# Optimization experiments

Measured on AMD Instinct MI355X. Metric: run time of the kernel, lower is better.

The kernel has to match this reference:

```python
import jax, jax.numpy as jnp
import numpy as np

GRID_SIZE = 5
GRID_RANGE = (-1.0, 1.0)


def setup_inputs() -> dict:
    key = jax.random.key(0)
    k1, k2, k3 = jax.random.split(key, 3)
    B, D, U, K = 16384, 1024, 128, GRID_SIZE + 3  # spline_order=3
    x = jax.random.normal(k1, (B, D), dtype=jnp.float32)
    # glorot-ish scale for weights
    base_weight = jax.random.normal(k2, (D, U), dtype=jnp.float32) * (1.0 / np.sqrt(D))
    spline_weight = jax.random.normal(k3, (D, U, K), dtype=jnp.float32) * (1.0 / np.sqrt(D))
    return {"x": x, "base_weight": base_weight, "spline_weight": spline_weight}


def reference(x, base_weight, spline_weight):
    # base path: SiLU(x @ W_b)
    base_out = jax.nn.silu(x @ base_weight)  # [B, U]
    # spline path: RBF over grid centers, then contract (note: x_norm in the
    # original call() is computed but unused, so it is omitted here)
    centers = jnp.linspace(GRID_RANGE[0], GRID_RANGE[1], GRID_SIZE)  # [G]
    dist = jnp.square(x[..., None] - centers)        # [B, D, G]
    rbf = jnp.exp(-5.0 * dist)                        # [B, D, G]
    spline_out = jnp.einsum('big,iug->bu', rbf, spline_weight[:, :, :GRID_SIZE])
    return base_out + spline_out
```

## Files before the change

### kernel.cpp

```cpp
#include <hip/hip_runtime.h>

typedef unsigned short u16;
typedef unsigned int u32;
typedef __bf16 bf16x8 __attribute__((ext_vector_type(8)));
typedef float f32x16 __attribute__((ext_vector_type(16)));

#define C2 (-7.213475204444817f)
#define T1C 0.28650480f
#define T2C 0.0067379470f

__device__ __forceinline__ u16 f2bf(float f) {
  u32 u = __float_as_uint(f);
  return (u16)((u + 0x7FFFu + ((u >> 16) & 1u)) >> 16);
}

__device__ __forceinline__ f32x16 mfma16(uint4 a, uint4 b, f32x16 c) {
  return __builtin_amdgcn_mfma_f32_32x32x16_bf16(
      __builtin_bit_cast(bf16x8, a), __builtin_bit_cast(bf16x8, b), c, 0, 0, 0);
}

__global__ __launch_bounds__(256) void kan_prep(const float* __restrict__ wb,
                                                const float* __restrict__ ws,
                                                u16* __restrict__ wst3) {
  __shared__ u16 tile[6][16][130];
  const int t = threadIdx.x;
  const int c = blockIdx.x;
#pragma unroll
  for (int it = 0; it < 8; ++it) {
    int idx = it * 256 + t;
    int d = idx >> 7, u = idx & 127;
    size_t base = (size_t)(c * 16 + d) * 128 + u;
    const float* p = ws + base * 8;
    float4 v0 = *(const float4*)p;
    float g4 = p[4];
    tile[0][d][u] = f2bf(v0.x);
    tile[1][d][u] = f2bf(v0.y);
    tile[2][d][u] = f2bf(v0.z);
    tile[3][d][u] = f2bf(v0.w);
    tile[4][d][u] = f2bf(g4);
    tile[5][d][u] = f2bf(wb[base]);
  }
  __syncthreads();
#pragma unroll
  for (int i = 0; i < 6; ++i) {
    int g = i * 256 + t;
    int s = g >> 8, r = g & 255;
    int nq = r >> 6, l = r & 63;
    int u = nq * 32 + (l & 31);
    int dbase = (l >> 5) * 8;
    u32 q[4];
#pragma unroll
    for (int j = 0; j < 4; ++j) {
      u32 lo = tile[s][dbase + 2 * j][u];
      u32 hi = tile[s][dbase + 2 * j + 1][u];
      q[j] = lo | (hi << 16);
    }
    uint4 w4; w4.x = q[0]; w4.y = q[1]; w4.z = q[2]; w4.w = q[3];
    *(uint4*)(wst3 + (size_t)c * 12288 + (size_t)g * 8) = w4;
  }
}

__global__ __launch_bounds__(512, 2) void kan_main(const float* __restrict__ x,
                                                   const u16* __restrict__ wst3,
                                                   float* __restrict__ out) {
  __shared__ __align__(16) char lds[98304];

  const int t = threadIdx.x;
  const int lane = t & 63;
  const int w = t >> 6;
  const int kq = w & 3;
  const int wn = w >> 2;
  const int b0 = blockIdx.x * 64;

  f32x16 acc[8];
#pragma unroll
  for (int i = 0; i < 8; ++i)
#pragma unroll
    for (int j = 0; j < 16; ++j) acc[i][j] = 0.f;

  const int r = t >> 3, o = t & 7;
  const float* xp = x + (size_t)(b0 + r) * 1024 + o * 8;
  const u32 aw = (u32)((((r >> 5) * 4 + (o >> 1)) << 10) + ((o & 1) << 9) +
                       (((r & 31) ^ o) << 4));

  const char* bsrc = (const char*)wst3 + kq * 24576 + wn * 2048 + lane * 16;

  const u32 ar = (u32)((kq << 10) + ((lane >> 5) << 9) +
                       ((((lane & 31) ^ (kq * 2 + (lane >> 5)))) << 4));

  auto rbf_write = [&](char* buf, float4 xa, float4 xb) {
    float xf[8] = {xa.x, xa.y, xa.z, xa.w, xb.x, xb.y, xb.z, xb.w};
    u32 pk[6][4];
#pragma unroll
    for (int pp = 0; pp < 4; ++pp) {
      u32 lo6[6], hi6[6];
#pragma unroll
      for (int e = 0; e < 2; ++e) {
        float xv = xf[2 * pp + e];
        float t0 = C2 * xv;
        float P = __builtin_amdgcn_exp2f(t0 * xv);
        float Qp = __builtin_amdgcn_exp2f(-t0);
        float Qm = __builtin_amdgcn_exp2f(t0);
        float PQ = P * Qp, PQm = P * Qm;
        u32* dst = e ? hi6 : lo6;
        dst[0] = __float_as_uint(PQm * Qm * T2C) + 0x8000u;
        dst[1] = __float_as_uint(PQm * T1C) + 0x8000u;
        dst[2] = __float_as_uint(P) + 0x8000u;
        dst[3] = __float_as_uint(PQ * T1C) + 0x8000u;
        dst[4] = __float_as_uint(PQ * Qp * T2C) + 0x8000u;
        dst[5] = __float_as_uint(xv) + 0x8000u;
      }
#pragma unroll
      for (int s = 0; s < 6; ++s)
        pk[s][pp] = __builtin_amdgcn_perm(hi6[s], lo6[s], 0x07060302);
    }
#pragma unroll
    for (int s = 0; s < 6; ++s) {
      uint4 v; v.x = pk[s][0]; v.y = pk[s][1]; v.z = pk[s][2]; v.w = pk[s][3];
      *(uint4*)(buf + s * 8192 + aw) = v;
    }
  };

  float4 xc0 = *(const float4*)(xp);
  float4 xc1 = *(const float4*)(xp + 4);
  rbf_write(lds, xc0, xc1);
  xc0 = *(const float4*)(xp + 64);
  xc1 = *(const float4*)(xp + 68);
  __syncthreads();

  for (int i = 0; i < 16; ++i) {
    char* cur = lds + (size_t)(i & 1) * 49152;
    char* nxt = lds + (size_t)((i + 1) & 1) * 49152;
    const char* bc = bsrc + (size_t)i * 98304;

    uint4 av[6], bv[6];
#pragma unroll
    for (int s = 0; s < 3; ++s) {
      bv[2 * s] = *(const uint4*)(bc + s * 4096);
      bv[2 * s + 1] = *(const uint4*)(bc + s * 4096 + 1024);
      av[2 * s] = *(const uint4*)(cur + s * 8192 + ar);
      av[2 * s + 1] = *(const uint4*)(cur + s * 8192 + 4096 + ar);
    }
    if (i < 15) {
      rbf_write(nxt, xc0, xc1);
      if (i < 14) {
        xc0 = *(const float4*)(xp + (i + 2) * 64);
        xc1 = *(const float4*)(xp + (i + 2) * 64 + 4);
      }
    }
#pragma unroll
    for (int s = 0; s < 3; ++s) {
      acc[0] = mfma16(av[2 * s], bv[2 * s], acc[0]);
      acc[1] = mfma16(av[2 * s], bv[2 * s + 1], acc[1]);
      acc[2] = mfma16(av[2 * s + 1], bv[2 * s], acc[2]);
      acc[3] = mfma16(av[2 * s + 1], bv[2 * s + 1], acc[3]);
    }
#pragma unroll
    for (int s = 3; s < 6; ++s) {
      int j = 2 * (s - 3);
      bv[j] = *(const uint4*)(bc + s * 4096);
      bv[j + 1] = *(const uint4*)(bc + s * 4096 + 1024);
      av[j] = *(const uint4*)(cur + s * 8192 + ar);
      av[j + 1] = *(const uint4*)(cur + s * 8192 + 4096 + ar);
    }
#pragma unroll
    for (int s = 3; s < 5; ++s) {
      int j = 2 * (s - 3);
      acc[0] = mfma16(av[j], bv[j], acc[0]);
      acc[1] = mfma16(av[j], bv[j + 1], acc[1]);
      acc[2] = mfma16(av[j + 1], bv[j], acc[2]);
      acc[3] = mfma16(av[j + 1], bv[j + 1], acc[3]);
    }
    acc[4] = mfma16(av[4], bv[4], acc[4]);
    acc[5] = mfma16(av[4], bv[5], acc[5]);
    acc[6] = mfma16(av[5], bv[4], acc[6]);
    acc[7] = mfma16(av[5], bv[5], acc[7]);
    __syncthreads();
  }

#pragma unroll
  for (int q = 0; q < 4; ++q) {
    if (kq != 0) {
      char* slab = lds + ((kq - 1) * 2 + wn) * 8192;
#pragma unroll
      for (int rq = 0; rq < 4; ++rq) {
        *(float4*)(slab + rq * 1024 + lane * 16) =
            make_float4(acc[q][4 * rq], acc[q][4 * rq + 1],
                        acc[q][4 * rq + 2], acc[q][4 * rq + 3]);
        *(float4*)(slab + 4096 + rq * 1024 + lane * 16) =
            make_float4(acc[4 + q][4 * rq], acc[4 + q][4 * rq + 1],
                        acc[4 + q][4 * rq + 2], acc[4 + q][4 * rq + 3]);
      }
    }
    __syncthreads();
    if (kq == 0) {
#pragma unroll
      for (int p = 1; p < 4; ++p) {
        const char* slab = lds + ((p - 1) * 2 + wn) * 8192;
#pragma unroll
        for (int rq = 0; rq < 4; ++rq) {
          float4 vs = *(const float4*)(slab + rq * 1024 + lane * 16);
          float4 vb = *(const float4*)(slab + 4096 + rq * 1024 + lane * 16);
          acc[q][4 * rq] += vs.x; acc[q][4 * rq + 1] += vs.y;
          acc[q][4 * rq + 2] += vs.z; acc[q][4 * rq + 3] += vs.w;
          acc[4 + q][4 * rq] += vb.x; acc[4 + q][4 * rq + 1] += vb.y;
          acc[4 + q][4 * rq + 2] += vb.z; acc[4 + q][4 * rq + 3] += vb.w;
        }
      }
      const int col = wn * 64 + (q & 1) * 32 + (lane & 31);
#pragma unroll
      for (int reg = 0; reg < 16; ++reg) {
        int row = (q >> 1) * 32 + (reg & 3) + 8 * (reg >> 2) + 4 * (lane >> 5);
        float z = acc[4 + q][reg];
        float sv = z / (1.0f + __expf(-z));
        out[(size_t)(b0 + row) * 128 + col] = sv + acc[q][reg];
      }
    }
    __syncthreads();
  }
}

extern "C" void kernel_launch(void* const* d_in, const int* in_sizes, int n_in,
                              void* d_out, int out_size, void* d_ws, size_t ws_size,
                              hipStream_t stream) {
  const float* x  = (const float*)d_in[0];
  const float* wb = (const float*)d_in[1];
  const float* ws = (const float*)d_in[2];
  u16* wst3 = (u16*)d_ws;
  float* out = (float*)d_out;

  kan_prep<<<dim3(64), 256, 0, stream>>>(wb, ws, wst3);
  kan_main<<<dim3(256), 512, 0, stream>>>(x, wst3, out);
}
```

Baseline: 137.3 us.

## Halve batch tile to 32 rows per block for more occupancy and staggered compute

Shrinks each block's batch tile from 64 to 32 rows, halving accumulators and LDS (48 KB) and doubling the grid to 512 blocks, with launch bounds raised to 4 blocks per CU. The MFMA inner loop becomes a software-pipelined chain that prefetches the next A/B fragments, and the two wave groups run the RBF generation and the GEMM in opposite order so VALU and matrix work overlap. This targets latency hiding through higher occupancy. The cost is that each block re-reads the full weight stream from global/L2 for half as many rows, so weight traffic per output doubles, and the tighter register budget may cause spills.

```diff
diff --git a/kernel.cpp b/kernel.cpp
--- a/kernel.cpp
+++ b/kernel.cpp
@@ -60,45 +60,45 @@
   }
 }
 
-__global__ __launch_bounds__(512, 2) void kan_main(const float* __restrict__ x,
+__global__ __launch_bounds__(512, 4) void kan_main(const float* __restrict__ x,
                                                    const u16* __restrict__ wst3,
                                                    float* __restrict__ out) {
-  __shared__ __align__(16) char lds[98304];
+  __shared__ __align__(16) char lds[49152];
 
   const int t = threadIdx.x;
   const int lane = t & 63;
   const int w = t >> 6;
   const int kq = w & 3;
   const int wn = w >> 2;
-  const int b0 = blockIdx.x * 64;
-
-  f32x16 acc[8];
-#pragma unroll
-  for (int i = 0; i < 8; ++i)
+  const int b0 = blockIdx.x * 32;
+
+  f32x16 acc[4];
+#pragma unroll
+  for (int i = 0; i < 4; ++i)
 #pragma unroll
     for (int j = 0; j < 16; ++j) acc[i][j] = 0.f;
 
-  const int r = t >> 3, o = t & 7;
-  const float* xp = x + (size_t)(b0 + r) * 1024 + o * 8;
-  const u32 aw = (u32)((((r >> 5) * 4 + (o >> 1)) << 10) + ((o & 1) << 9) +
-                       (((r & 31) ^ o) << 4));
+  const int r = t >> 4, o4 = t & 15;
+  const float* xp = x + (size_t)(b0 + r) * 1024 + o4 * 4;
+  const u32 aw = ((u32)(o4 >> 2) << 10) + ((u32)((o4 >> 1) & 1) << 9) +
+                 ((u32)((r ^ (o4 >> 1)) & 31) << 4) + ((u32)(o4 & 1) << 3);
 
   const char* bsrc = (const char*)wst3 + kq * 24576 + wn * 2048 + lane * 16;
 
-  const u32 ar = (u32)((kq << 10) + ((lane >> 5) << 9) +
-                       ((((lane & 31) ^ (kq * 2 + (lane >> 5)))) << 4));
-
-  auto rbf_write = [&](char* buf, float4 xa, float4 xb) {
-    float xf[8] = {xa.x, xa.y, xa.z, xa.w, xb.x, xb.y, xb.z, xb.w};
-    u32 pk[6][4];
-#pragma unroll
-    for (int pp = 0; pp < 4; ++pp) {
+  const u32 ar = ((u32)kq << 10) + ((u32)(lane >> 5) << 9) +
+                 ((u32)((lane & 31) ^ (kq * 2 + (lane >> 5))) << 4);
+
+  auto rbf_write = [&](char* buf, float4 xv) {
+    float xf[4] = {xv.x, xv.y, xv.z, xv.w};
+    u32 pk[6][2];
+#pragma unroll
+    for (int pp = 0; pp < 2; ++pp) {
       u32 lo6[6], hi6[6];
 #pragma unroll
       for (int e = 0; e < 2; ++e) {
-        float xv = xf[2 * pp + e];
-        float t0 = C2 * xv;
-        float P = __builtin_amdgcn_exp2f(t0 * xv);
+        float v = xf[2 * pp + e];
+        float t0 = C2 * v;
+        float P = __builtin_amdgcn_exp2f(t0 * v);
         float Qp = __builtin_amdgcn_exp2f(-t0);
         float Qm = __builtin_amdgcn_exp2f(t0);
         float PQ = P * Qp, PQm = P * Qm;
@@ -108,7 +108,7 @@
         dst[2] = __float_as_uint(P) + 0x8000u;
         dst[3] = __float_as_uint(PQ * T1C) + 0x8000u;
         dst[4] = __float_as_uint(PQ * Qp * T2C) + 0x8000u;
-        dst[5] = __float_as_uint(xv) + 0x8000u;
+        dst[5] = __float_as_uint(v) + 0x8000u;
       }
 #pragma unroll
       for (int s = 0; s < 6; ++s)
@@ -116,70 +116,65 @@
     }
 #pragma unroll
     for (int s = 0; s < 6; ++s) {
-      uint4 v; v.x = pk[s][0]; v.y = pk[s][1]; v.z = pk[s][2]; v.w = pk[s][3];
-      *(uint4*)(buf + s * 8192 + aw) = v;
+      uint2 v2; v2.x = pk[s][0]; v2.y = pk[s][1];
+      *(uint2*)(buf + s * 4096 + aw) = v2;
     }
   };
 
-  float4 xc0 = *(const float4*)(xp);
-  float4 xc1 = *(const float4*)(xp + 4);
-  rbf_write(lds, xc0, xc1);
-  xc0 = *(const float4*)(xp + 64);
-  xc1 = *(const float4*)(xp + 68);
+  auto gemm_chain = [&](const char* cur, const char* bp) {
+    uint4 a0 = *(const uint4*)(cur + ar);
+    uint4 c0 = *(const uint4*)(bp);
+    uint4 c1 = *(const uint4*)(bp + 1024);
+    uint4 a1 = *(const uint4*)(cur + 4096 + ar);
+    uint4 c2 = *(const uint4*)(bp + 4096);
+    uint4 c3 = *(const uint4*)(bp + 4096 + 1024);
+#pragma unroll
+    for (int s = 0; s < 6; ++s) {
+      uint4 au = a0, b0 = c0, b1 = c1;
+      a0 = a1; c0 = c2; c1 = c3;
+      if (s < 4) {
+        a1 = *(const uint4*)(cur + (s + 2) * 4096 + ar);
+        c2 = *(const uint4*)(bp + (s + 2) * 4096);
+        c3 = *(const uint4*)(bp + (s + 2) * 4096 + 1024);
+      }
+      if (s < 5) {
+        acc[0] = mfma16(au, b0, acc[0]);
+        acc[1] = mfma16(au, b1, acc[1]);
+      } else {
+        acc[2] = mfma16(au, b0, acc[2]);
+        acc[3] = mfma16(au, b1, acc[3]);
+      }
+    }
+  };
+
+  float4 xc = *(const float4*)xp;
+  rbf_write(lds, xc);
+  xc = *(const float4*)(xp + 64);
   __syncthreads();
 
   for (int i = 0; i < 16; ++i) {
-    char* cur = lds + (size_t)(i & 1) * 49152;
-    char* nxt = lds + (size_t)((i + 1) & 1) * 49152;
+    char* cur = lds + (i & 1) * 24576;
+    char* nxt = lds + ((i + 1) & 1) * 24576;
     const char* bc = bsrc + (size_t)i * 98304;
 
-    uint4 av[6], bv[6];
-#pragma unroll
-    for (int s = 0; s < 3; ++s) {
-      bv[2 * s] = *(const uint4*)(bc + s * 4096);
-      bv[2 * s + 1] = *(const uint4*)(bc + s * 4096 + 1024);
-      av[2 * s] = *(const uint4*)(cur + s * 8192 + ar);
-      av[2 * s + 1] = *(const uint4*)(cur + s * 8192 + 4096 + ar);
-    }
-    if (i < 15) {
-      rbf_write(nxt, xc0, xc1);
-      if (i < 14) {
-        xc0 = *(const float4*)(xp + (i + 2) * 64);
-        xc1 = *(const float4*)(xp + (i + 2) * 64 + 4);
-      }
-    }
-#pragma unroll
-    for (int s = 0; s < 3; ++s) {
-      acc[0] = mfma16(av[2 * s], bv[2 * s], acc[0]);
-      acc[1] = mfma16(av[2 * s], bv[2 * s + 1], acc[1]);
-      acc[2] = mfma16(av[2 * s + 1], bv[2 * s], acc[2]);
-      acc[3] = mfma16(av[2 * s + 1], bv[2 * s + 1], acc[3]);
-    }
-#pragma unroll
-    for (int s = 3; s < 6; ++s) {
-      int j = 2 * (s - 3);
-      bv[j] = *(const uint4*)(bc + s * 4096);
-      bv[j + 1] = *(const uint4*)(bc + s * 4096 + 1024);
-      av[j] = *(const uint4*)(cur + s * 8192 + ar);
-      av[j + 1] = *(const uint4*)(cur + s * 8192 + 4096 + ar);
-    }
-#pragma unroll
-    for (int s = 3; s < 5; ++s) {
-      int j = 2 * (s - 3);
-      acc[0] = mfma16(av[j], bv[j], acc[0]);
-      acc[1] = mfma16(av[j], bv[j + 1], acc[1]);
-      acc[2] = mfma16(av[j + 1], bv[j], acc[2]);
-      acc[3] = mfma16(av[j + 1], bv[j + 1], acc[3]);
-    }
-    acc[4] = mfma16(av[4], bv[4], acc[4]);
-    acc[5] = mfma16(av[4], bv[5], acc[5]);
-    acc[6] = mfma16(av[5], bv[4], acc[6]);
-    acc[7] = mfma16(av[5], bv[5], acc[7]);
+    if (wn == 0) {
+      if (i < 15) {
+        rbf_write(nxt, xc);
+        if (i < 14) xc = *(const float4*)(xp + (i + 2) * 64);
+      }
+      gemm_chain(cur, bc);
+    } else {
+      gemm_chain(cur, bc);
+      if (i < 15) {
+        rbf_write(nxt, xc);
+        if (i < 14) xc = *(const float4*)(xp + (i + 2) * 64);
+      }
+    }
     __syncthreads();
   }
 
 #pragma unroll
-  for (int q = 0; q < 4; ++q) {
+  for (int q = 0; q < 2; ++q) {
     if (kq != 0) {
       char* slab = lds + ((kq - 1) * 2 + wn) * 8192;
 #pragma unroll
@@ -188,8 +183,8 @@
             make_float4(acc[q][4 * rq], acc[q][4 * rq + 1],
                         acc[q][4 * rq + 2], acc[q][4 * rq + 3]);
         *(float4*)(slab + 4096 + rq * 1024 + lane * 16) =
-            make_float4(acc[4 + q][4 * rq], acc[4 + q][4 * rq + 1],
-                        acc[4 + q][4 * rq + 2], acc[4 + q][4 * rq + 3]);
+            make_float4(acc[2 + q][4 * rq], acc[2 + q][4 * rq + 1],
+                        acc[2 + q][4 * rq + 2], acc[2 + q][4 * rq + 3]);
       }
     }
     __syncthreads();
@@ -203,15 +198,15 @@
           float4 vb = *(const float4*)(slab + 4096 + rq * 1024 + lane * 16);
           acc[q][4 * rq] += vs.x; acc[q][4 * rq + 1] += vs.y;
           acc[q][4 * rq + 2] += vs.z; acc[q][4 * rq + 3] += vs.w;
-          acc[4 + q][4 * rq] += vb.x; acc[4 + q][4 * rq + 1] += vb.y;
-          acc[4 + q][4 * rq + 2] += vb.z; acc[4 + q][4 * rq + 3] += vb.w;
+          acc[2 + q][4 * rq] += vb.x; acc[2 + q][4 * rq + 1] += vb.y;
+          acc[2 + q][4 * rq + 2] += vb.z; acc[2 + q][4 * rq + 3] += vb.w;
         }
       }
-      const int col = wn * 64 + (q & 1) * 32 + (lane & 31);
+      const int col = wn * 64 + q * 32 + (lane & 31);
 #pragma unroll
       for (int reg = 0; reg < 16; ++reg) {
-        int row = (q >> 1) * 32 + (reg & 3) + 8 * (reg >> 2) + 4 * (lane >> 5);
-        float z = acc[4 + q][reg];
+        int row = (reg & 3) + 8 * (reg >> 2) + 4 * (lane >> 5);
+        float z = acc[2 + q][reg];
         float sv = z / (1.0f + __expf(-z));
         out[(size_t)(b0 + row) * 128 + col] = sv + acc[q][reg];
       }
@@ -230,5 +225,5 @@
   float* out = (float*)d_out;
 
   kan_prep<<<dim3(64), 256, 0, stream>>>(wb, ws, wst3);
-  kan_main<<<dim3(256), 512, 0, stream>>>(x, wst3, out);
-}
+  kan_main<<<dim3(512), 512, 0, stream>>>(x, wst3, out);
+}
```

New measurement: 170.4 us. 24.1% more time.

## Stage raw x into LDS asynchronously and build RBF fragments in registers

Applied to the files above, without the earlier changes.

Raw x tiles are now copied straight into LDS with global_load_lds, double-buffered over 8 iterations. Each wave reads its own x slice and computes the RBF/bf16 fragments in registers, so the bf16 A-operand round trip through LDS is gone. Each K-quarter wave group now walks a contiguous 256-wide d range of the packed weights instead of interleaved chunks, and the LDS footprint shrinks. The cost is that the exp work is duplicated across the two column-half waves that share rows.

```diff
diff --git a/kernel.cpp b/kernel.cpp
--- a/kernel.cpp
+++ b/kernel.cpp
@@ -63,7 +63,7 @@
 __global__ __launch_bounds__(512, 2) void kan_main(const float* __restrict__ x,
                                                    const u16* __restrict__ wst3,
                                                    float* __restrict__ out) {
-  __shared__ __align__(16) char lds[98304];
+  __shared__ __align__(16) char lds[65536];
 
   const int t = threadIdx.x;
   const int lane = t & 63;
@@ -78,17 +78,29 @@
 #pragma unroll
     for (int j = 0; j < 16; ++j) acc[i][j] = 0.f;
 
-  const int r = t >> 3, o = t & 7;
-  const float* xp = x + (size_t)(b0 + r) * 1024 + o * 8;
-  const u32 aw = (u32)((((r >> 5) * 4 + (o >> 1)) << 10) + ((o & 1) << 9) +
-                       (((r & 31) ^ o) << 4));
-
-  const char* bsrc = (const char*)wst3 + kq * 24576 + wn * 2048 + lane * 16;
-
-  const u32 ar = (u32)((kq << 10) + ((lane >> 5) << 9) +
-                       ((((lane & 31) ^ (kq * 2 + (lane >> 5)))) << 4));
-
-  auto rbf_write = [&](char* buf, float4 xa, float4 xb) {
+  const int srow = t >> 3, sq = t & 7;
+  const float* xsrc =
+      x + (size_t)(b0 + srow) * 1024 + (size_t)((sq ^ (srow & 7)) * 4);
+
+  auto stage = [&](char* buf, int body) {
+    const float* s0 = xsrc + body * 32;
+#pragma unroll
+    for (int rr = 0; rr < 4; ++rr) {
+      __builtin_amdgcn_global_load_lds(
+          (const __attribute__((address_space(1))) u32*)(s0 + rr * 256),
+          (__attribute__((address_space(3))) u32*)(buf + rr * 8192 + w * 1024),
+          16, 0, 0);
+    }
+  };
+
+  const int rrow = lane & 31;
+  const int kh = lane >> 5;
+  const int rs = rrow & 7;
+
+  const char* bsrc =
+      (const char*)wst3 + (size_t)kq * 393216 + wn * 2048 + lane * 16;
+
+  auto mkfrag = [&](const float4& xa, const float4& xb, uint4* fr) {
     float xf[8] = {xa.x, xa.y, xa.z, xa.w, xb.x, xb.y, xb.z, xb.w};
     u32 pk[6][4];
 #pragma unroll
@@ -116,65 +128,52 @@
     }
 #pragma unroll
     for (int s = 0; s < 6; ++s) {
-      uint4 v; v.x = pk[s][0]; v.y = pk[s][1]; v.z = pk[s][2]; v.w = pk[s][3];
-      *(uint4*)(buf + s * 8192 + aw) = v;
+      fr[s].x = pk[s][0]; fr[s].y = pk[s][1];
+      fr[s].z = pk[s][2]; fr[s].w = pk[s][3];
     }
   };
 
-  float4 xc0 = *(const float4*)(xp);
-  float4 xc1 = *(const float4*)(xp + 4);
-  rbf_write(lds, xc0, xc1);
-  xc0 = *(const float4*)(xp + 64);
-  xc1 = *(const float4*)(xp + 68);
+  stage(lds, 0);
   __syncthreads();
 
-  for (int i = 0; i < 16; ++i) {
-    char* cur = lds + (size_t)(i & 1) * 49152;
-    char* nxt = lds + (size_t)((i + 1) & 1) * 49152;
-    const char* bc = bsrc + (size_t)i * 98304;
-
-    uint4 av[6], bv[6];
-#pragma unroll
-    for (int s = 0; s < 3; ++s) {
-      bv[2 * s] = *(const uint4*)(bc + s * 4096);
-      bv[2 * s + 1] = *(const uint4*)(bc + s * 4096 + 1024);
-      av[2 * s] = *(const uint4*)(cur + s * 8192 + ar);
-      av[2 * s + 1] = *(const uint4*)(cur + s * 8192 + 4096 + ar);
-    }
-    if (i < 15) {
-      rbf_write(nxt, xc0, xc1);
-      if (i < 14) {
-        xc0 = *(const float4*)(xp + (i + 2) * 64);
-        xc1 = *(const float4*)(xp + (i + 2) * 64 + 4);
-      }
-    }
-#pragma unroll
-    for (int s = 0; s < 3; ++s) {
-      acc[0] = mfma16(av[2 * s], bv[2 * s], acc[0]);
-      acc[1] = mfma16(av[2 * s], bv[2 * s + 1], acc[1]);
-      acc[2] = mfma16(av[2 * s + 1], bv[2 * s], acc[2]);
-      acc[3] = mfma16(av[2 * s + 1], bv[2 * s + 1], acc[3]);
-    }
-#pragma unroll
-    for (int s = 3; s < 6; ++s) {
-      int j = 2 * (s - 3);
-      bv[j] = *(const uint4*)(bc + s * 4096);
-      bv[j + 1] = *(const uint4*)(bc + s * 4096 + 1024);
-      av[j] = *(const uint4*)(cur + s * 8192 + ar);
-      av[j + 1] = *(const uint4*)(cur + s * 8192 + 4096 + ar);
-    }
-#pragma unroll
-    for (int s = 3; s < 5; ++s) {
-      int j = 2 * (s - 3);
-      acc[0] = mfma16(av[j], bv[j], acc[0]);
-      acc[1] = mfma16(av[j], bv[j + 1], acc[1]);
-      acc[2] = mfma16(av[j + 1], bv[j], acc[2]);
-      acc[3] = mfma16(av[j + 1], bv[j + 1], acc[3]);
-    }
-    acc[4] = mfma16(av[4], bv[4], acc[4]);
-    acc[5] = mfma16(av[4], bv[5], acc[5]);
-    acc[6] = mfma16(av[5], bv[4], acc[6]);
-    acc[7] = mfma16(av[5], bv[5], acc[7]);
+  for (int i = 0; i < 8; ++i) {
+    char* cur = lds + (i & 1) * 32768;
+    char* nxt = lds + ((i + 1) & 1) * 32768;
+    if (i < 7) stage(nxt, i + 1);
+
+#pragma unroll
+    for (int cc = 0; cc < 2; ++cc) {
+      const char* bc = bsrc + (size_t)(i * 2 + cc) * 24576;
+      uint4 b0v[6], b1v[6];
+#pragma unroll
+      for (int s = 0; s < 6; ++s) {
+        b0v[s] = *(const uint4*)(bc + s * 4096);
+        b1v[s] = *(const uint4*)(bc + s * 4096 + 1024);
+      }
+      const char* wbase = cur + kq * 8192;
+      const int q0 = cc * 4 + kh * 2;
+      const int sA = q0 ^ rs, sB = (q0 + 1) ^ rs;
+      const char* r0 = wbase + rrow * 128;
+      const char* r1 = wbase + (32 + rrow) * 128;
+      float4 xa0 = *(const float4*)(r0 + sA * 16);
+      float4 xb0 = *(const float4*)(r0 + sB * 16);
+      float4 xa1 = *(const float4*)(r1 + sA * 16);
+      float4 xb1 = *(const float4*)(r1 + sB * 16);
+      uint4 fa[6], fb[6];
+      mkfrag(xa0, xb0, fa);
+      mkfrag(xa1, xb1, fb);
+#pragma unroll
+      for (int s = 0; s < 5; ++s) {
+        acc[0] = mfma16(fa[s], b0v[s], acc[0]);
+        acc[1] = mfma16(fa[s], b1v[s], acc[1]);
+        acc[2] = mfma16(fb[s], b0v[s], acc[2]);
+        acc[3] = mfma16(fb[s], b1v[s], acc[3]);
+      }
+      acc[4] = mfma16(fa[5], b0v[5], acc[4]);
+      acc[5] = mfma16(fa[5], b1v[5], acc[5]);
+      acc[6] = mfma16(fb[5], b0v[5], acc[6]);
+      acc[7] = mfma16(fb[5], b1v[5], acc[7]);
+    }
     __syncthreads();
   }
 
```

After: 137.2 us. About the same (-0.1%).

## Warp-specialize main kernel into RBF producer and MFMA consumer warps

Applied to the files above, without the earlier changes.

The main kernel now splits its eight waves into two roles. Four producer waves compute the RBF features into double-buffered LDS, and four consumer waves each own a 32-column slice, looping over the full K range with MFMA. Because every consumer covers all of K, the cross-wave split-K reduction through LDS at the end goes away, and s_setprio is added around the MFMA bursts. The cost is that each consumer wave issues more MFMAs and B loads, and the producers no longer help with matrix work.

```diff
diff --git a/kernel.cpp b/kernel.cpp
--- a/kernel.cpp
+++ b/kernel.cpp
@@ -68,155 +68,136 @@
   const int t = threadIdx.x;
   const int lane = t & 63;
   const int w = t >> 6;
-  const int kq = w & 3;
-  const int wn = w >> 2;
   const int b0 = blockIdx.x * 64;
 
-  f32x16 acc[8];
-#pragma unroll
-  for (int i = 0; i < 8; ++i)
-#pragma unroll
-    for (int j = 0; j < 16; ++j) acc[i][j] = 0.f;
-
-  const int r = t >> 3, o = t & 7;
-  const float* xp = x + (size_t)(b0 + r) * 1024 + o * 8;
-  const u32 aw = (u32)((((r >> 5) * 4 + (o >> 1)) << 10) + ((o & 1) << 9) +
-                       (((r & 31) ^ o) << 4));
-
-  const char* bsrc = (const char*)wst3 + kq * 24576 + wn * 2048 + lane * 16;
-
-  const u32 ar = (u32)((kq << 10) + ((lane >> 5) << 9) +
-                       ((((lane & 31) ^ (kq * 2 + (lane >> 5)))) << 4));
-
-  auto rbf_write = [&](char* buf, float4 xa, float4 xb) {
-    float xf[8] = {xa.x, xa.y, xa.z, xa.w, xb.x, xb.y, xb.z, xb.w};
-    u32 pk[6][4];
-#pragma unroll
-    for (int pp = 0; pp < 4; ++pp) {
-      u32 lo6[6], hi6[6];
-#pragma unroll
-      for (int e = 0; e < 2; ++e) {
-        float xv = xf[2 * pp + e];
-        float t0 = C2 * xv;
-        float P = __builtin_amdgcn_exp2f(t0 * xv);
-        float Qp = __builtin_amdgcn_exp2f(-t0);
-        float Qm = __builtin_amdgcn_exp2f(t0);
-        float PQ = P * Qp, PQm = P * Qm;
-        u32* dst = e ? hi6 : lo6;
-        dst[0] = __float_as_uint(PQm * Qm * T2C) + 0x8000u;
-        dst[1] = __float_as_uint(PQm * T1C) + 0x8000u;
-        dst[2] = __float_as_uint(P) + 0x8000u;
-        dst[3] = __float_as_uint(PQ * T1C) + 0x8000u;
-        dst[4] = __float_as_uint(PQ * Qp * T2C) + 0x8000u;
-        dst[5] = __float_as_uint(xv) + 0x8000u;
-      }
-#pragma unroll
-      for (int s = 0; s < 6; ++s)
-        pk[s][pp] = __builtin_amdgcn_perm(hi6[s], lo6[s], 0x07060302);
-    }
-#pragma unroll
-    for (int s = 0; s < 6; ++s) {
-      uint4 v; v.x = pk[s][0]; v.y = pk[s][1]; v.z = pk[s][2]; v.w = pk[s][3];
-      *(uint4*)(buf + s * 8192 + aw) = v;
-    }
-  };
-
-  float4 xc0 = *(const float4*)(xp);
-  float4 xc1 = *(const float4*)(xp + 4);
-  rbf_write(lds, xc0, xc1);
-  xc0 = *(const float4*)(xp + 64);
-  xc1 = *(const float4*)(xp + 68);
-  __syncthreads();
-
-  for (int i = 0; i < 16; ++i) {
-    char* cur = lds + (size_t)(i & 1) * 49152;
-    char* nxt = lds + (size_t)((i + 1) & 1) * 49152;
-    const char* bc = bsrc + (size_t)i * 98304;
-
-    uint4 av[6], bv[6];
-#pragma unroll
-    for (int s = 0; s < 3; ++s) {
-      bv[2 * s] = *(const uint4*)(bc + s * 4096);
-      bv[2 * s + 1] = *(const uint4*)(bc + s * 4096 + 1024);
-      av[2 * s] = *(const uint4*)(cur + s * 8192 + ar);
-      av[2 * s + 1] = *(const uint4*)(cur + s * 8192 + 4096 + ar);
-    }
-    if (i < 15) {
-      rbf_write(nxt, xc0, xc1);
-      if (i < 14) {
-        xc0 = *(const float4*)(xp + (i + 2) * 64);
-        xc1 = *(const float4*)(xp + (i + 2) * 64 + 4);
-      }
-    }
-#pragma unroll
-    for (int s = 0; s < 3; ++s) {
-      acc[0] = mfma16(av[2 * s], bv[2 * s], acc[0]);
-      acc[1] = mfma16(av[2 * s], bv[2 * s + 1], acc[1]);
-      acc[2] = mfma16(av[2 * s + 1], bv[2 * s], acc[2]);
-      acc[3] = mfma16(av[2 * s + 1], bv[2 * s + 1], acc[3]);
-    }
-#pragma unroll
-    for (int s = 3; s < 6; ++s) {
-      int j = 2 * (s - 3);
-      bv[j] = *(const uint4*)(bc + s * 4096);
-      bv[j + 1] = *(const uint4*)(bc + s * 4096 + 1024);
-      av[j] = *(const uint4*)(cur + s * 8192 + ar);
-      av[j + 1] = *(const uint4*)(cur + s * 8192 + 4096 + ar);
-    }
-#pragma unroll
-    for (int s = 3; s < 5; ++s) {
-      int j = 2 * (s - 3);
-      acc[0] = mfma16(av[j], bv[j], acc[0]);
-      acc[1] = mfma16(av[j], bv[j + 1], acc[1]);
-      acc[2] = mfma16(av[j + 1], bv[j], acc[2]);
-      acc[3] = mfma16(av[j + 1], bv[j + 1], acc[3]);
-    }
-    acc[4] = mfma16(av[4], bv[4], acc[4]);
-    acc[5] = mfma16(av[4], bv[5], acc[5]);
-    acc[6] = mfma16(av[5], bv[4], acc[6]);
-    acc[7] = mfma16(av[5], bv[5], acc[7]);
+  if (w < 4) {
+    const int pid = (w << 6) + lane;
+    const int r0 = pid >> 3;
+    const int o = pid & 7;
+    const u32 aw0 = ((u32)(o >> 1) << 10) + ((u32)(o & 1) << 9) +
+                    ((u32)((r0 ^ o) & 31) << 4);
+    const u32 aw1 = aw0 + 4096;
+    const float* xpA = x + (size_t)(b0 + r0) * 1024 + o * 8;
+    const float* xpB = xpA + 32 * 1024;
+
+    auto rbf6 = [&](char* buf, u32 aw, float4 xa, float4 xb) {
+      float xf[8] = {xa.x, xa.y, xa.z, xa.w, xb.x, xb.y, xb.z, xb.w};
+      u32 pk[6][4];
+#pragma unroll
+      for (int pp = 0; pp < 4; ++pp) {
+        u32 lo6[6], hi6[6];
+#pragma unroll
+        for (int e = 0; e < 2; ++e) {
+          float xv = xf[2 * pp + e];
+          float t0 = C2 * xv;
+          float P = __builtin_amdgcn_exp2f(t0 * xv);
+          float Qp = __builtin_amdgcn_exp2f(-t0);
+          float Qm = __builtin_amdgcn_exp2f(t0);
+          float PQ = P * Qp, PQm = P * Qm;
+          u32* dst = e ? hi6 : lo6;
+          dst[0] = __float_as_uint(PQm * Qm * T2C) + 0x8000u;
+          dst[1] = __float_as_uint(PQm * T1C) + 0x8000u;
+          dst[2] = __float_as_uint(P) + 0x8000u;
+          dst[3] = __float_as_uint(PQ * T1C) + 0x8000u;
+          dst[4] = __float_as_uint(PQ * Qp * T2C) + 0x8000u;
+          dst[5] = __float_as_uint(xv) + 0x8000u;
+        }
+#pragma unroll
+        for (int s = 0; s < 6; ++s)
+          pk[s][pp] = __builtin_amdgcn_perm(hi6[s], lo6[s], 0x07060302);
+      }
+#pragma unroll
+      for (int s = 0; s < 6; ++s) {
+        uint4 v; v.x = pk[s][0]; v.y = pk[s][1]; v.z = pk[s][2]; v.w = pk[s][3];
+        *(uint4*)(buf + s * 8192 + aw) = v;
+      }
+    };
+
+    float4 xA0 = *(const float4*)(xpA);
+    float4 xA1 = *(const float4*)(xpA + 4);
+    float4 xB0 = *(const float4*)(xpB);
+    float4 xB1 = *(const float4*)(xpB + 4);
+    rbf6(lds, aw0, xA0, xA1);
+    rbf6(lds, aw1, xB0, xB1);
+    xA0 = *(const float4*)(xpA + 64);
+    xA1 = *(const float4*)(xpA + 68);
+    xB0 = *(const float4*)(xpB + 64);
+    xB1 = *(const float4*)(xpB + 68);
     __syncthreads();
-  }
-
-#pragma unroll
-  for (int q = 0; q < 4; ++q) {
-    if (kq != 0) {
-      char* slab = lds + ((kq - 1) * 2 + wn) * 8192;
-#pragma unroll
-      for (int rq = 0; rq < 4; ++rq) {
-        *(float4*)(slab + rq * 1024 + lane * 16) =
-            make_float4(acc[q][4 * rq], acc[q][4 * rq + 1],
-                        acc[q][4 * rq + 2], acc[q][4 * rq + 3]);
-        *(float4*)(slab + 4096 + rq * 1024 + lane * 16) =
-            make_float4(acc[4 + q][4 * rq], acc[4 + q][4 * rq + 1],
-                        acc[4 + q][4 * rq + 2], acc[4 + q][4 * rq + 3]);
-      }
-    }
+
+    for (int i = 0; i < 16; ++i) {
+      if (i < 15) {
+        char* nxt = lds + ((i + 1) & 1) * 49152;
+        rbf6(nxt, aw0, xA0, xA1);
+        rbf6(nxt, aw1, xB0, xB1);
+        if (i < 14) {
+          xA0 = *(const float4*)(xpA + (i + 2) * 64);
+          xA1 = *(const float4*)(xpA + (i + 2) * 64 + 4);
+          xB0 = *(const float4*)(xpB + (i + 2) * 64);
+          xB1 = *(const float4*)(xpB + (i + 2) * 64 + 4);
+        }
+      }
+      __syncthreads();
+    }
+  } else {
+    const int wn = w - 4;
+    const int kh = lane >> 5;
+    u32 aoff[4];
+#pragma unroll
+    for (int p = 0; p < 4; ++p)
+      aoff[p] = (u32)(p * 1024 + kh * 512 +
+                      ((((lane & 31) ^ (p * 2 + kh)) & 31) << 4));
+    const char* bb = (const char*)wst3 + wn * 1024 + lane * 16;
+
+    f32x16 acc[4];
+#pragma unroll
+    for (int i = 0; i < 4; ++i)
+#pragma unroll
+      for (int j = 0; j < 16; ++j) acc[i][j] = 0.f;
+
     __syncthreads();
-    if (kq == 0) {
-#pragma unroll
-      for (int p = 1; p < 4; ++p) {
-        const char* slab = lds + ((p - 1) * 2 + wn) * 8192;
-#pragma unroll
-        for (int rq = 0; rq < 4; ++rq) {
-          float4 vs = *(const float4*)(slab + rq * 1024 + lane * 16);
-          float4 vb = *(const float4*)(slab + 4096 + rq * 1024 + lane * 16);
-          acc[q][4 * rq] += vs.x; acc[q][4 * rq + 1] += vs.y;
-          acc[q][4 * rq + 2] += vs.z; acc[q][4 * rq + 3] += vs.w;
-          acc[4 + q][4 * rq] += vb.x; acc[4 + q][4 * rq + 1] += vb.y;
-          acc[4 + q][4 * rq + 2] += vb.z; acc[4 + q][4 * rq + 3] += vb.w;
-        }
-      }
-      const int col = wn * 64 + (q & 1) * 32 + (lane & 31);
+
+    for (int i = 0; i < 16; ++i) {
+      const char* cur = lds + (i & 1) * 49152;
+      uint4 bv[4][6];
+#pragma unroll
+      for (int p = 0; p < 4; ++p)
+#pragma unroll
+        for (int s = 0; s < 6; ++s)
+          bv[p][s] =
+              *(const uint4*)(bb + (size_t)(i * 4 + p) * 24576 + s * 4096);
+#pragma unroll
+      for (int p = 0; p < 4; ++p) {
+        uint4 a0[6], a1[6];
+#pragma unroll
+        for (int s = 0; s < 6; ++s) {
+          a0[s] = *(const uint4*)(cur + s * 8192 + aoff[p]);
+          a1[s] = *(const uint4*)(cur + s * 8192 + 4096 + aoff[p]);
+        }
+        __builtin_amdgcn_s_setprio(1);
+#pragma unroll
+        for (int s = 0; s < 5; ++s) {
+          acc[0] = mfma16(a0[s], bv[p][s], acc[0]);
+          acc[1] = mfma16(a1[s], bv[p][s], acc[1]);
+        }
+        acc[2] = mfma16(a0[5], bv[p][5], acc[2]);
+        acc[3] = mfma16(a1[5], bv[p][5], acc[3]);
+        __builtin_amdgcn_s_setprio(0);
+      }
+      __syncthreads();
+    }
+
+    const int col = wn * 32 + (lane & 31);
+#pragma unroll
+    for (int g = 0; g < 2; ++g) {
 #pragma unroll
       for (int reg = 0; reg < 16; ++reg) {
-        int row = (q >> 1) * 32 + (reg & 3) + 8 * (reg >> 2) + 4 * (lane >> 5);
-        float z = acc[4 + q][reg];
+        int row = g * 32 + (reg & 3) + 8 * (reg >> 2) + 4 * (lane >> 5);
+        float z = acc[2 + g][reg];
         float sv = z / (1.0f + __expf(-z));
-        out[(size_t)(b0 + row) * 128 + col] = sv + acc[q][reg];
-      }
-    }
-    __syncthreads();
+        out[(size_t)(b0 + row) * 128 + col] = sv + acc[g][reg];
+      }
+    }
   }
 }
 
```

After: 124.2 us. -9.5%, faster.
